# Kernel tuning notes

Measured on AMD Instinct MI355X. Metric: run time of the kernel, lower is better.

The kernel has to match this reference:

```python
import jax, jax.numpy as jnp
import numpy as np

S = 16          # state_dim
H = 96          # hidden_dim
A = 64          # num_actions
B = 256         # batch_size
D_IN = S * S * 64      # 16384
D_H = H * H            # 9216
SPLIT = D_H - S * S    # 8960, action/selection split point


def setup_inputs() -> dict:
    key = jax.random.key(0)
    ks = jax.random.split(key, 14)
    s = jax.random.normal(ks[0], (B, S, S, 64), dtype=jnp.float32)
    mask = jax.random.randint(ks[1], (B, S, S), 0, 2).astype(bool)
    u = jax.random.uniform(ks[2], (B, S * S), dtype=jnp.float32,
                           minval=1e-6, maxval=1.0 - 1e-6)
    def lin(k, fin, fout):
        kw, kb = jax.random.split(k)
        sc = 1.0 / np.sqrt(fin)
        return (jax.random.uniform(kw, (fin, fout), minval=-sc, maxval=sc, dtype=jnp.float32),
                jax.random.uniform(kb, (fout,), minval=-sc, maxval=sc, dtype=jnp.float32))
    W1, b1 = lin(ks[3], D_IN, D_H)
    W2, b2 = lin(ks[4], D_H, D_H)
    W3, b3 = lin(ks[5], D_H, D_H)
    Wa, ba = lin(ks[6], SPLIT, A)
    Ws, bs = lin(ks[7], S * S, S * S)
    return {"s": s, "mask": mask, "u": u, "W1": W1, "b1": b1, "W2": W2,
            "b2": b2, "W3": W3, "b3": b3, "Wa": Wa, "ba": ba, "Ws": Ws, "bs": bs}


def reference(s, mask, u, W1, b1, W2, b2, W3, b3, Wa, ba, Ws, bs):
    x = s.reshape(s.shape[0], -1).astype(jnp.float32)        # [B, D_IN]
    x = jax.nn.relu(x @ W1 + b1)                             # [B, D_H]
    x = jax.nn.relu(x @ W2 + b2)
    x = jax.nn.relu(x @ W3 + b3)
    x_action = jax.nn.softmax(x[:, :SPLIT] @ Wa + ba, axis=1)  # [B, A]
    # selection branch
    p = jax.nn.softmax(x[:, SPLIT:] @ Ws + bs, axis=1)         # [B, S*S]
    m = mask.reshape(mask.shape[0], -1)                        # [B, S*S]
    p = jnp.where(m, -1e9, p)        # masked_fill on the probs (faithful)
    p = jax.nn.softmax(p, axis=1)
    # parallel Gumbel-max == Categorical over valid (unnormalized) probs
    gumbel = -jnp.log(-jnp.log(u))
    scores = jnp.where(m, -jnp.inf, jnp.log(p) + gumbel)
    idx = jnp.argmax(scores, axis=1)                           # [B]
    coordinate = jnp.stack([idx // S, idx % S], axis=1)        # [B, 2]
    sel_prob = jnp.take_along_axis(p, idx[:, None], axis=1)    # [B, 1]
    final_action_prob = x_action * sel_prob                    # [B, A]
    return final_action_prob, coordinate
```

## Files before the change

kernel.cpp:

```cpp
#include <hip/hip_runtime.h>
#include <hip/hip_fp16.h>


typedef _Float16 f16;
typedef _Float16 f16x4 __attribute__((ext_vector_type(4)));
typedef _Float16 f16x8 __attribute__((ext_vector_type(8)));
typedef float f32x4 __attribute__((ext_vector_type(4)));

#define DH 9216
#define SPLIT 8960

__device__ __forceinline__ void gload16(const void* g, void* l) {
    __builtin_amdgcn_global_load_lds(
        (const __attribute__((address_space(1))) void*)g,
        (__attribute__((address_space(3))) void*)l, 16, 0, 0);
}

__device__ __forceinline__ size_t pk_off(int row, int k) {
    int tk = k >> 5, q = (k >> 3) & 3;
    int mhalf = row >> 7, wmA = (row >> 6) & 1, ri = (row >> 4) & 3, lc = row & 15;
    int h = (wmA << 8) | (ri << 6) | (q << 4) | lc;
    return (size_t)(tk * 2 + mhalf) * 8192 + (size_t)h * 16;
}

__global__ void cvt_kernel(const float* __restrict__ in, char* __restrict__ outp) {
    int idx = blockIdx.x * blockDim.x + threadIdx.x;
    int row = idx >> 11;
    int k8  = (idx & 2047) << 3;
    const float* src = in + ((size_t)row << 14) + k8;
    f16x8 h;
#pragma unroll
    for (int j = 0; j < 8; ++j) h[j] = (_Float16)src[j];
    *(f16x8*)(outp + pk_off(row, k8)) = h;
}

__global__ __launch_bounds__(256, 2) void gemm_kernel(
    const char* __restrict__ Ap, int K, int Kh, int yshift,
    const float* __restrict__ W,
    f16* __restrict__ P)
{
    __shared__ __align__(16) char lds[2][32768];
    const int bid  = blockIdx.x;
    const int y    = bid & ((1 << yshift) - 1);
    const int n0   = (bid >> yshift) << 7;
    const int tid  = threadIdx.x;
    const int lane = tid & 63;
    const int wid  = tid >> 6;
    const int wm   = wid >> 1, wn = wid & 1;
    const int kbase = y * Kh;
    const int ns   = Kh >> 5;

    f32x4 acc[8][4] = {};

    const float* wsrc0;
    const float* wsrc1;
    const float* wsrc2;
    const float* wsrc3;
    {
        int g0 = tid,      k0 = g0 >> 5, c0 = (g0 & 31) ^ ((5 * (k0 >> 3)) & 31);
        int g1 = tid + 256, k1 = g1 >> 5, c1 = (g1 & 31) ^ ((5 * (k1 >> 3)) & 31);
        int g2 = tid + 512, k2 = g2 >> 5, c2 = (g2 & 31) ^ ((5 * (k2 >> 3)) & 31);
        int g3 = tid + 768, k3 = g3 >> 5, c3 = (g3 & 31) ^ ((5 * (k3 >> 3)) & 31);
        wsrc0 = W + (size_t)(kbase + k0) * DH + n0 + (c0 << 2);
        wsrc1 = W + (size_t)(kbase + k1) * DH + n0 + (c1 << 2);
        wsrc2 = W + (size_t)(kbase + k2) * DH + n0 + (c2 << 2);
        wsrc3 = W + (size_t)(kbase + k3) * DH + n0 + (c3 << 2);
    }
    const char* ap = Ap + (size_t)(y * (Kh >> 5) * 2) * 8192;

    auto issue = [&](int slot) {
        char* dst = &lds[slot][0];
        gload16(wsrc0, dst + (size_t)tid * 16);          wsrc0 += 32 * DH;
        gload16(wsrc1, dst + (size_t)(tid + 256) * 16);  wsrc1 += 32 * DH;
        gload16(wsrc2, dst + (size_t)(tid + 512) * 16);  wsrc2 += 32 * DH;
        gload16(wsrc3, dst + (size_t)(tid + 768) * 16);  wsrc3 += 32 * DH;
        gload16(ap + (size_t)tid * 16,         dst + 16384 + (size_t)tid * 16);
        gload16(ap + (size_t)tid * 16 + 4096,  dst + 16384 + (size_t)tid * 16 + 4096);
        gload16(ap + (size_t)tid * 16 + 8192,  dst + 16384 + (size_t)tid * 16 + 8192);
        gload16(ap + (size_t)tid * 16 + 12288, dst + 16384 + (size_t)tid * 16 + 12288);
        ap += 16384;
    };

    const int q  = lane >> 4;
    const int lc = lane & 15;
    auto step = [&](int slot) {
        const float* wl = (const float*)&lds[slot][0];
        const f16*   al = (const f16*)&lds[slot][16384];
        f16x8 af[8], bf[4];
#pragma unroll
        for (int ri8 = 0; ri8 < 8; ++ri8) {
            int off = (wm << 12) + (((ri8 >> 2) << 8) | ((ri8 & 3) << 6)) + lane;
            af[ri8] = *(const f16x8*)(al + ((size_t)off << 3));
        }
        const int wbase = (q << 10) + (lc & 3);
#pragma unroll
        for (int ni = 0; ni < 4; ++ni) {
            int p = ((wn << 4) + (ni << 2) + (lc >> 2)) ^ (5 * q);
            int fi = wbase + ((p & 31) << 2);
            f16x8 b;
#pragma unroll
            for (int j = 0; j < 8; ++j)
                b[j] = (_Float16)wl[fi + (j << 7)];
            bf[ni] = b;
        }
#pragma unroll
        for (int ri = 0; ri < 8; ++ri)
#pragma unroll
            for (int ni = 0; ni < 4; ++ni)
                acc[ri][ni] = __builtin_amdgcn_mfma_f32_16x16x32_f16(
                    af[ri], bf[ni], acc[ri][ni], 0, 0, 0);
    };

    issue(0);
    issue(1);
    __builtin_amdgcn_sched_barrier(0);

    for (int t = 0; t < ns; ++t) {
        if (t + 1 < ns) asm volatile("s_waitcnt vmcnt(8)" ::: "memory");
        else            asm volatile("s_waitcnt vmcnt(0)" ::: "memory");
        __builtin_amdgcn_sched_barrier(0);
        __builtin_amdgcn_s_barrier();
        __builtin_amdgcn_sched_barrier(0);
        step(t & 1);
        __builtin_amdgcn_sched_barrier(0);
        asm volatile("s_waitcnt lgkmcnt(0)" ::: "memory");
        __builtin_amdgcn_sched_barrier(0);
        __builtin_amdgcn_s_barrier();
        __builtin_amdgcn_sched_barrier(0);
        if (t + 2 < ns) {
            issue(t & 1);
            __builtin_amdgcn_sched_barrier(0);
        }
    }

    f16* Pb = P + (size_t)y * (256 * DH);
#pragma unroll
    for (int ri = 0; ri < 8; ++ri) {
        int row = wm * 128 + ri * 16 + (q << 2);
#pragma unroll
        for (int ni = 0; ni < 4; ++ni) {
            int col = n0 + wn * 64 + ni * 16 + lc;
#pragma unroll
            for (int rg = 0; rg < 4; ++rg)
                Pb[(size_t)(row + rg) * DH + col] = (_Float16)acc[ri][ni][rg];
        }
    }
}

__global__ __launch_bounds__(256) void reduce_kernel(
    const f16* __restrict__ P, int S,
    const float* __restrict__ bias,
    char* __restrict__ ohp, float* __restrict__ out32) {
    const size_t n = 256 * DH;
    const size_t i = ((size_t)blockIdx.x * 256 + threadIdx.x) * 8;
    if (i >= n) return;
    const int row = (int)(i / DH);
    const int d   = (int)(i % DH);
    float r[8];
    {
        float4 b0 = *(const float4*)(bias + d);
        float4 b1 = *(const float4*)(bias + d + 4);
        r[0] = b0.x; r[1] = b0.y; r[2] = b0.z; r[3] = b0.w;
        r[4] = b1.x; r[5] = b1.y; r[6] = b1.z; r[7] = b1.w;
    }
    for (int j = 0; j < S; ++j) {
        f16x8 v = *(const f16x8*)(P + (size_t)j * n + i);
#pragma unroll
        for (int e = 0; e < 8; ++e) r[e] += (float)v[e];
    }
#pragma unroll
    for (int e = 0; e < 8; ++e) r[e] = fmaxf(r[e], 0.f);
    if (ohp) {
        f16x8 h;
#pragma unroll
        for (int e = 0; e < 8; ++e) h[e] = (_Float16)r[e];
        *(f16x8*)(ohp + pk_off(row, d)) = h;
    }
    if (out32) {
        float4 o0 = {r[0], r[1], r[2], r[3]};
        float4 o1 = {r[4], r[5], r[6], r[7]};
        *(float4*)(out32 + i) = o0;
        *(float4*)(out32 + i + 4) = o1;
    }
}

__global__ __launch_bounds__(256) void action_kernel(
    const float* __restrict__ X3, const float* __restrict__ Wa,
    const float* __restrict__ ba, float* __restrict__ xact) {
    __shared__ float xs[SPLIT];
    __shared__ float red[256];
    const int row = blockIdx.x, t = threadIdx.x;
    const float* xr = X3 + (size_t)row * DH;
    for (int k = t * 4; k < SPLIT; k += 1024)
        *(float4*)&xs[k] = *(const float4*)(xr + k);
    __syncthreads();
    const int col = t & 63, kqq = t >> 6;
    float acc = 0.f;
    for (int k = kqq * 2240; k < (kqq + 1) * 2240; ++k)
        acc += xs[k] * Wa[(size_t)k * 64 + col];
    red[t] = acc;
    __syncthreads();
    if (t < 64) {
        float z = red[t] + red[t + 64] + red[t + 128] + red[t + 192] + ba[t];
        float mx = z;
        for (int off = 32; off; off >>= 1) mx = fmaxf(mx, __shfl_xor(mx, off));
        float e = expf(z - mx);
        float s = e;
        for (int off = 32; off; off >>= 1) s += __shfl_xor(s, off);
        xact[row * 64 + t] = e / s;
    }
}

__global__ __launch_bounds__(256) void select_kernel(
    const float* __restrict__ X3, const float* __restrict__ Ws,
    const float* __restrict__ bs, const void* __restrict__ maskp,
    const float* __restrict__ u, const float* __restrict__ xact,
    float* __restrict__ out) {
    __shared__ float xs[256];
    __shared__ float psh[256];
    __shared__ float rr[4];
    __shared__ float bestv[4];
    __shared__ int besti[4];
    __shared__ int sIdx;
    __shared__ int smode;
    const int row = blockIdx.x, t = threadIdx.x;
    const int lane = t & 63, wid = t >> 6;

    if (t < 64) {
        unsigned v = ((const unsigned*)maskp)[t];
        int okInt  = __all(v <= 1u);
        int okByte = __all((v & 0xFEFEFEFEu) == 0u);
        if (t == 0) smode = okInt ? 0 : (okByte ? 1 : 2);
    }
    xs[t] = X3[(size_t)row * DH + SPLIT + t];
    __syncthreads();

    bool mk;
    if (smode == 0)       mk = ((const int*)maskp)[row * 256 + t] != 0;
    else if (smode == 1)  mk = ((const unsigned char*)maskp)[row * 256 + t] != 0;
    else                  mk = ((const float*)maskp)[row * 256 + t] != 0.0f;

    float z = bs[t];
    for (int k = 0; k < 256; ++k)
        z += xs[k] * Ws[k * 256 + t];

    float v = z;
    for (int off = 32; off; off >>= 1) v = fmaxf(v, __shfl_xor(v, off));
    if (lane == 0) rr[wid] = v;
    __syncthreads();
    float m1 = fmaxf(fmaxf(rr[0], rr[1]), fmaxf(rr[2], rr[3]));
    __syncthreads();
    float e1 = expf(z - m1);
    v = e1;
    for (int off = 32; off; off >>= 1) v += __shfl_xor(v, off);
    if (lane == 0) rr[wid] = v;
    __syncthreads();
    float s1 = rr[0] + rr[1] + rr[2] + rr[3];
    __syncthreads();
    float p1 = e1 / s1;

    float q = mk ? -1e9f : p1;
    v = q;
    for (int off = 32; off; off >>= 1) v = fmaxf(v, __shfl_xor(v, off));
    if (lane == 0) rr[wid] = v;
    __syncthreads();
    float m2 = fmaxf(fmaxf(rr[0], rr[1]), fmaxf(rr[2], rr[3]));
    __syncthreads();
    float e2 = expf(q - m2);
    v = e2;
    for (int off = 32; off; off >>= 1) v += __shfl_xor(v, off);
    if (lane == 0) rr[wid] = v;
    __syncthreads();
    float s2 = rr[0] + rr[1] + rr[2] + rr[3];
    float p2 = e2 / s2;
    psh[t] = p2;

    float g = -logf(-logf(u[row * 256 + t]));
    float sc = mk ? -INFINITY : (logf(p2) + g);
    float bv = sc;
    int bi = t;
    for (int off = 32; off; off >>= 1) {
        float ov = __shfl_xor(bv, off);
        int oi = __shfl_xor(bi, off);
        if (ov > bv || (ov == bv && oi < bi)) { bv = ov; bi = oi; }
    }
    if (lane == 0) { bestv[wid] = bv; besti[wid] = bi; }
    __syncthreads();
    if (t == 0) {
        float fv = bestv[0];
        int fi = besti[0];
        for (int w = 1; w < 4; ++w)
            if (bestv[w] > fv || (bestv[w] == fv && besti[w] < fi)) {
                fv = bestv[w]; fi = besti[w];
            }
        sIdx = fi;
    }
    __syncthreads();
    const int idx = sIdx;
    const float sp = psh[idx];
    if (t < 64) out[row * 64 + t] = xact[row * 64 + t] * sp;
    if (t == 0) {
        out[256 * 64 + row * 2 + 0] = (float)(idx >> 4);
        out[256 * 64 + row * 2 + 1] = (float)(idx & 15);
    }
}

extern "C" void kernel_launch(void* const* d_in, const int* in_sizes, int n_in,
                              void* d_out, int out_size, void* d_ws, size_t ws_size,
                              hipStream_t stream) {
    const float* s  = (const float*)d_in[0];
    const void*  mask = d_in[1];
    const float* u  = (const float*)d_in[2];
    const float* W1 = (const float*)d_in[3];
    const float* b1 = (const float*)d_in[4];
    const float* W2 = (const float*)d_in[5];
    const float* b2 = (const float*)d_in[6];
    const float* W3 = (const float*)d_in[7];
    const float* b3 = (const float*)d_in[8];
    const float* Wa = (const float*)d_in[9];
    const float* ba = (const float*)d_in[10];
    const float* Ws = (const float*)d_in[11];
    const float* bs = (const float*)d_in[12];
    float* out = (float*)d_out;
    char* ws = (char*)d_ws;

    char*  A0p = ws + 0;
    char*  X1p = ws + 8388608;
    char*  X2p = ws + 0;
    float* X3  = (float*)(ws + 13107200);
    float* XA  = (float*)(ws + 22544384);
    f16*   P   = (f16*)(ws + 22609920);

    const size_t pbytes = 4718592ull;
    int yshift = (ws_size >= 22609920ull + 16 * pbytes) ? 4 : 3;
    const int S = 1 << yshift;

    cvt_kernel<<<2048, 256, 0, stream>>>(s, A0p);

    const int nblk = 72 << yshift;
    gemm_kernel<<<nblk, 256, 0, stream>>>(A0p, 16384, 16384 / S, yshift, W1, P);
    reduce_kernel<<<1152, 256, 0, stream>>>(P, S, b1, X1p, nullptr);
    gemm_kernel<<<nblk, 256, 0, stream>>>(X1p, DH, DH / S, yshift, W2, P);
    reduce_kernel<<<1152, 256, 0, stream>>>(P, S, b2, X2p, nullptr);
    gemm_kernel<<<nblk, 256, 0, stream>>>(X2p, DH, DH / S, yshift, W3, P);
    reduce_kernel<<<1152, 256, 0, stream>>>(P, S, b3, nullptr, X3);

    action_kernel<<<256, 256, 0, stream>>>(X3, Wa, ba, XA);
    select_kernel<<<256, 256, 0, stream>>>(X3, Ws, bs, mask, u, XA, out);
}
```

Measured before the change: 509.8 us.

## Fuse last split-K reduction with action and selection heads; halve split factor

Removes the separate third reduce kernel and the action and select kernels. A single per-row tail kernel now sums the layer-3 split-K partials, applies bias and ReLU into shared memory, and computes both heads from there. This drops the fp32 X3 round trip through global memory and two kernel launches. The workspace layout also changes, so the split-K factor falls from 16/8 to 8/4. That halves the partial-sum traffic but gives each GEMM fewer blocks, with longer K loops per block.

Result: faster. 495.3 us (-2.8%).

```diff
diff --git a/kernel.cpp b/kernel.cpp
--- a/kernel.cpp
+++ b/kernel.cpp
@@ -150,7 +150,7 @@
 __global__ __launch_bounds__(256) void reduce_kernel(
     const f16* __restrict__ P, int S,
     const float* __restrict__ bias,
-    char* __restrict__ ohp, float* __restrict__ out32) {
+    char* __restrict__ ohp) {
     const size_t n = 256 * DH;
     const size_t i = ((size_t)blockIdx.x * 256 + threadIdx.x) * 8;
     if (i >= n) return;
@@ -170,53 +170,21 @@
     }
 #pragma unroll
     for (int e = 0; e < 8; ++e) r[e] = fmaxf(r[e], 0.f);
-    if (ohp) {
-        f16x8 h;
-#pragma unroll
-        for (int e = 0; e < 8; ++e) h[e] = (_Float16)r[e];
-        *(f16x8*)(ohp + pk_off(row, d)) = h;
-    }
-    if (out32) {
-        float4 o0 = {r[0], r[1], r[2], r[3]};
-        float4 o1 = {r[4], r[5], r[6], r[7]};
-        *(float4*)(out32 + i) = o0;
-        *(float4*)(out32 + i + 4) = o1;
-    }
-}
-
-__global__ __launch_bounds__(256) void action_kernel(
-    const float* __restrict__ X3, const float* __restrict__ Wa,
-    const float* __restrict__ ba, float* __restrict__ xact) {
-    __shared__ float xs[SPLIT];
+    f16x8 h;
+#pragma unroll
+    for (int e = 0; e < 8; ++e) h[e] = (_Float16)r[e];
+    *(f16x8*)(ohp + pk_off(row, d)) = h;
+}
+
+__global__ __launch_bounds__(256) void tail_kernel(
+    const f16* __restrict__ P, int S, const float* __restrict__ b3,
+    const float* __restrict__ Wa, const float* __restrict__ ba,
+    const float* __restrict__ Ws, const float* __restrict__ bs,
+    const void* __restrict__ maskp, const float* __restrict__ u,
+    float* __restrict__ out) {
+    __shared__ float xrow[DH];
     __shared__ float red[256];
-    const int row = blockIdx.x, t = threadIdx.x;
-    const float* xr = X3 + (size_t)row * DH;
-    for (int k = t * 4; k < SPLIT; k += 1024)
-        *(float4*)&xs[k] = *(const float4*)(xr + k);
-    __syncthreads();
-    const int col = t & 63, kqq = t >> 6;
-    float acc = 0.f;
-    for (int k = kqq * 2240; k < (kqq + 1) * 2240; ++k)
-        acc += xs[k] * Wa[(size_t)k * 64 + col];
-    red[t] = acc;
-    __syncthreads();
-    if (t < 64) {
-        float z = red[t] + red[t + 64] + red[t + 128] + red[t + 192] + ba[t];
-        float mx = z;
-        for (int off = 32; off; off >>= 1) mx = fmaxf(mx, __shfl_xor(mx, off));
-        float e = expf(z - mx);
-        float s = e;
-        for (int off = 32; off; off >>= 1) s += __shfl_xor(s, off);
-        xact[row * 64 + t] = e / s;
-    }
-}
-
-__global__ __launch_bounds__(256) void select_kernel(
-    const float* __restrict__ X3, const float* __restrict__ Ws,
-    const float* __restrict__ bs, const void* __restrict__ maskp,
-    const float* __restrict__ u, const float* __restrict__ xact,
-    float* __restrict__ out) {
-    __shared__ float xs[256];
+    __shared__ float xact[64];
     __shared__ float psh[256];
     __shared__ float rr[4];
     __shared__ float bestv[4];
@@ -225,6 +193,7 @@
     __shared__ int smode;
     const int row = blockIdx.x, t = threadIdx.x;
     const int lane = t & 63, wid = t >> 6;
+    const size_t n = 256 * DH;
 
     if (t < 64) {
         unsigned v = ((const unsigned*)maskp)[t];
@@ -232,8 +201,42 @@
         int okByte = __all((v & 0xFEFEFEFEu) == 0u);
         if (t == 0) smode = okInt ? 0 : (okByte ? 1 : 2);
     }
-    xs[t] = X3[(size_t)row * DH + SPLIT + t];
-    __syncthreads();
+
+    for (int base = t * 8; base < DH; base += 2048) {
+        float r[8];
+        float4 b0 = *(const float4*)(b3 + base);
+        float4 b1 = *(const float4*)(b3 + base + 4);
+        r[0] = b0.x; r[1] = b0.y; r[2] = b0.z; r[3] = b0.w;
+        r[4] = b1.x; r[5] = b1.y; r[6] = b1.z; r[7] = b1.w;
+        const size_t idx = (size_t)row * DH + base;
+        for (int j = 0; j < S; ++j) {
+            f16x8 v = *(const f16x8*)(P + (size_t)j * n + idx);
+#pragma unroll
+            for (int e = 0; e < 8; ++e) r[e] += (float)v[e];
+        }
+#pragma unroll
+        for (int e = 0; e < 8; ++e) xrow[base + e] = fmaxf(r[e], 0.f);
+    }
+    __syncthreads();
+
+    {
+        const int col = t & 63, kqq = t >> 6;
+        float acc = 0.f;
+        for (int k = kqq * 2240; k < (kqq + 1) * 2240; ++k)
+            acc += xrow[k] * Wa[(size_t)k * 64 + col];
+        red[t] = acc;
+        __syncthreads();
+        if (t < 64) {
+            float z = red[t] + red[t + 64] + red[t + 128] + red[t + 192] + ba[t];
+            float mx = z;
+            for (int off = 32; off; off >>= 1) mx = fmaxf(mx, __shfl_xor(mx, off));
+            float e = expf(z - mx);
+            float s = e;
+            for (int off = 32; off; off >>= 1) s += __shfl_xor(s, off);
+            xact[t] = e / s;
+        }
+        __syncthreads();
+    }
 
     bool mk;
     if (smode == 0)       mk = ((const int*)maskp)[row * 256 + t] != 0;
@@ -242,7 +245,7 @@
 
     float z = bs[t];
     for (int k = 0; k < 256; ++k)
-        z += xs[k] * Ws[k * 256 + t];
+        z += xrow[SPLIT + k] * Ws[k * 256 + t];
 
     float v = z;
     for (int off = 32; off; off >>= 1) v = fmaxf(v, __shfl_xor(v, off));
@@ -298,7 +301,7 @@
     __syncthreads();
     const int idx = sIdx;
     const float sp = psh[idx];
-    if (t < 64) out[row * 64 + t] = xact[row * 64 + t] * sp;
+    if (t < 64) out[row * 64 + t] = xact[t] * sp;
     if (t == 0) {
         out[256 * 64 + row * 2 + 0] = (float)(idx >> 4);
         out[256 * 64 + row * 2 + 1] = (float)(idx & 15);
@@ -327,24 +330,20 @@
     char*  A0p = ws + 0;
     char*  X1p = ws + 8388608;
     char*  X2p = ws + 0;
-    float* X3  = (float*)(ws + 13107200);
-    float* XA  = (float*)(ws + 22544384);
-    f16*   P   = (f16*)(ws + 22609920);
+    f16*   P   = (f16*)(ws + 13107200);
 
     const size_t pbytes = 4718592ull;
-    int yshift = (ws_size >= 22609920ull + 16 * pbytes) ? 4 : 3;
+    int yshift = (ws_size >= 13107200ull + 8 * pbytes) ? 3 : 2;
     const int S = 1 << yshift;
 
     cvt_kernel<<<2048, 256, 0, stream>>>(s, A0p);
 
     const int nblk = 72 << yshift;
     gemm_kernel<<<nblk, 256, 0, stream>>>(A0p, 16384, 16384 / S, yshift, W1, P);
-    reduce_kernel<<<1152, 256, 0, stream>>>(P, S, b1, X1p, nullptr);
+    reduce_kernel<<<1152, 256, 0, stream>>>(P, S, b1, X1p);
     gemm_kernel<<<nblk, 256, 0, stream>>>(X1p, DH, DH / S, yshift, W2, P);
-    reduce_kernel<<<1152, 256, 0, stream>>>(P, S, b2, X2p, nullptr);
+    reduce_kernel<<<1152, 256, 0, stream>>>(P, S, b2, X2p);
     gemm_kernel<<<nblk, 256, 0, stream>>>(X2p, DH, DH / S, yshift, W3, P);
-    reduce_kernel<<<1152, 256, 0, stream>>>(P, S, b3, nullptr, X3);
-
-    action_kernel<<<256, 256, 0, stream>>>(X3, Wa, ba, XA);
-    select_kernel<<<256, 256, 0, stream>>>(X3, Ws, bs, mask, u, XA, out);
-}
+
+    tail_kernel<<<256, 256, 0, stream>>>(P, S, b3, Wa, ba, Ws, bs, mask, u, out);
+}
```
